# Kernel optimization log

Hardware: AMD Instinct MI355X
Metric: run time of the kernel (lower is better)

Reference implementation:

```python
import jax, jax.numpy as jnp
import numpy as np

FEA_DIM = 256
NUM_HEADS = 8
B, N = 32, 48


def setup_inputs() -> dict:
    key = jax.random.key(0)
    ks = jax.random.split(key, 30)
    d = FEA_DIM
    inp = {
        "async_fea": jax.random.normal(ks[0], (B, N, d), dtype=jnp.float32),
        "sync_fea": jax.random.normal(ks[1], (B, N, d), dtype=jnp.float32),
        "async_adj": jax.random.randint(ks[2], (B, N, N), 0, 2, dtype=jnp.int32),
        "sync_adj": jax.random.randint(ks[3], (B, N, N), 0, 2, dtype=jnp.int32),
    }
    i = 4
    for pref in ("a_", "s_"):
        for nm in ("Wq", "Wk", "Wv", "Wo", "Wm"):
            inp[pref + nm] = 0.02 * jax.random.normal(ks[i], (d, d), dtype=jnp.float32); i += 1
            inp[pref + nm.replace("W", "b")] = 0.02 * jax.random.normal(ks[i], (d,), dtype=jnp.float32); i += 1
    return inp


def _aggregate(x_src, adj, fallback, Wq, bq, Wk, bk, Wv, bv, Wo, bo, Wm, bm):
    """For each target t: self-attention among neighbor set {s : adj[b,s,t] > 0}
    of x_src, mean-pool over neighbors, divide by count again, linear map.
    Targets with no neighbors fall back to `fallback`."""
    Bb, Nn, D = x_src.shape
    H = NUM_HEADS
    dh = D // H
    q = (x_src @ Wq.T + bq).reshape(Bb, Nn, H, dh)
    k = (x_src @ Wk.T + bk).reshape(Bb, Nn, H, dh)
    v = (x_src @ Wv.T + bv).reshape(Bb, Nn, H, dh)
    # shared pairwise scores among source nodes: [B, H, Q, K]
    scores = jnp.einsum("bqhd,bkhd->bhqk", q, k) / jnp.sqrt(jnp.float32(dh))
    # neighbor mask per target: adj[b, s, t] > 0 -> m[b, t, s]
    m = jnp.transpose(adj > 0, (0, 2, 1))  # [B, T, S] bool
    # per-target masked softmax over keys: logits [B, T, H, Q, K]
    key_bias = jnp.where(m[:, :, None, None, :], 0.0, -1e9)
    attn = jax.nn.softmax(scores[:, None] + key_bias, axis=-1)  # [B,T,H,Q,K]
    out = jnp.einsum("bthqk,bkhd->bthqd", attn, v).reshape(Bb, Nn, Nn, D)  # [B,T,Q,D]
    out = out @ Wo.T + bo
    mf = m.astype(out.dtype)  # [B, T, Q]
    cnt = mf.sum(-1)  # [B, T]
    denom = jnp.maximum(cnt, 1.0)
    # torch: mean over valid queries, then / edge_cnt  => sum / cnt^2
    pooled = jnp.einsum("btq,btqd->btd", mf, out) / (denom * denom)[..., None]
    mapped = pooled @ Wm.T + bm
    return jnp.where((cnt > 0)[..., None], mapped, fallback)


def reference(async_fea, sync_fea, async_adj, sync_adj,
              a_Wq, a_bq, a_Wk, a_bk, a_Wv, a_bv, a_Wo, a_bo, a_Wm, a_bm,
              s_Wq, s_bq, s_Wk, s_bk, s_Wv, s_bv, s_Wo, s_bo, s_Wm, s_bm):
    refined_async = _aggregate(sync_fea, sync_adj, async_fea,
                               a_Wq, a_bq, a_Wk, a_bk, a_Wv, a_bv, a_Wo, a_bo, a_Wm, a_bm)
    refined_sync = _aggregate(async_fea, async_adj, sync_fea,
                              s_Wq, s_bq, s_Wk, s_bk, s_Wv, s_bv, s_Wo, s_bo, s_Wm, s_bm)
    return jnp.concatenate([refined_async, refined_sync, async_fea, sync_fea], axis=2)
```

## Files before the change

kernel.cpp:

```cpp
#include <hip/hip_runtime.h>

typedef __attribute__((ext_vector_type(8))) short short8v;
typedef __attribute__((ext_vector_type(4))) float f32x4;
typedef unsigned short u16t;

__device__ __forceinline__ u16t f2bf(float f) {
    union { float f; unsigned u; } v; v.f = f;
    unsigned u = v.u;
    return (u16t)((u + 0x7FFFu + ((u >> 16) & 1u)) >> 16);
}
__device__ __forceinline__ float bf2f(u16t u) {
    union { unsigned u; float f; } v; v.u = ((unsigned)u) << 16; return v.f;
}
__device__ __forceinline__ short8v cvt8(const float* p) {
    float4 lo = *(const float4*)p;
    float4 hi = *(const float4*)(p + 4);
    union { uint4 u; short8v s; } r;
    asm("v_cvt_pk_bf16_f32 %0, %1, %2" : "=v"(r.u.x) : "v"(lo.x), "v"(lo.y));
    asm("v_cvt_pk_bf16_f32 %0, %1, %2" : "=v"(r.u.y) : "v"(lo.z), "v"(lo.w));
    asm("v_cvt_pk_bf16_f32 %0, %1, %2" : "=v"(r.u.z) : "v"(hi.x), "v"(hi.y));
    asm("v_cvt_pk_bf16_f32 %0, %1, %2" : "=v"(r.u.w) : "v"(hi.z), "v"(hi.w));
    return r.s;
}
__device__ __forceinline__ short8v ld52(const u16t* p) {
    union { uint2 u[2]; short8v s; } r;
    r.u[0] = *(const uint2*)(p);
    r.u[1] = *(const uint2*)(p + 4);
    return r.s;
}

struct Params {
    const float *async_fea, *sync_fea;
    const int *async_adj, *sync_adj;
    const float *Wf[10];
    const float *bqkv[6];
    const float *bo_[2], *bm_[2];
    u16t *Wb;
    u16t *Qb, *Kb;
    u16t *VTg;
    u16t *Eg, *ETg;
    float *out;
};

__global__ __launch_bounds__(256) void convert_kernel(Params p)
{
    int g8 = (blockIdx.x * 256 + threadIdx.x) * 8;
    int w = g8 >> 16;
    int off = g8 & 65535;
    *(short8v*)(p.Wb + g8) = cvt8(p.Wf[w] + off);
}

__global__ __launch_bounds__(256) void qkv_kernel(Params p)
{
    int bid = blockIdx.x;
    int xcd = bid & 7, idx = bid >> 3;
    int agg = xcd >> 2, xcd_in = xcd & 3;
    int ct = idx % 12, rt = (idx / 12) * 4 + xcd_in;
    int wave = threadIdx.x >> 6, lane = threadIdx.x & 63;
    int l15 = lane & 15, g = lane >> 4;
    int row0 = rt * 64 + wave * 16;
    int mat = ct >> 2;
    int cbase = (ct & 3) * 64;
    const float* X = agg ? p.async_fea : p.sync_fea;
    const float* Xp = X + (row0 + l15) * 256 + g * 8;
    const u16t* Wp = p.Wb + (agg * 5 + mat) * 65536 + (cbase + l15) * 256 + g * 8;
    f32x4 acc[4] = {{0,0,0,0},{0,0,0,0},{0,0,0,0},{0,0,0,0}};
    #pragma unroll
    for (int kk = 0; kk < 8; ++kk) {
        short8v a = cvt8(Xp + kk * 32);
        #pragma unroll
        for (int j = 0; j < 4; ++j) {
            short8v b = *(const short8v*)(Wp + j * 16 * 256 + kk * 32);
            acc[j] = __builtin_amdgcn_mfma_f32_16x16x32_bf16(a, b, acc[j], 0, 0, 0);
        }
    }
    const float* bias = p.bqkv[agg * 3 + mat];
    if (mat < 2) {
        u16t* dst = ((mat == 0) ? p.Qb : p.Kb) + agg * 393216;
        #pragma unroll
        for (int j = 0; j < 4; ++j) {
            int c = cbase + j * 16 + l15;
            float bv = bias[c];
            #pragma unroll
            for (int i = 0; i < 4; ++i) {
                int row = row0 + g * 4 + i;
                dst[row * 256 + c] = f2bf(acc[j][i] + bv);
            }
        }
    } else {
        u16t* vt = p.VTg + agg * 393216;
        #pragma unroll
        for (int j = 0; j < 4; ++j) {
            int c = cbase + j * 16 + l15;
            float bv = bias[c];
            #pragma unroll
            for (int i = 0; i < 4; ++i) {
                int row = row0 + g * 4 + i;
                vt[(row / 48) * 12288 + c * 48 + (row % 48)] = f2bf(acc[j][i] + bv);
            }
        }
    }
}

__global__ __launch_bounds__(192) void scores_kernel(Params p)
{
    int bid = blockIdx.x;
    int xcd = bid & 7, idx = bid >> 3;
    int agg = xcd >> 2, xcd_in = xcd & 3;
    int h = idx & 7, b = (idx >> 3) * 4 + xcd_in;
    int qt = threadIdx.x >> 6, lane = threadIdx.x & 63;
    int l15 = lane & 15, g = lane >> 4;
    const u16t* Qp = p.Qb + agg * 393216 + (b * 48 + qt * 16 + l15) * 256 + h * 32 + g * 8;
    short8v a = *(const short8v*)Qp;
    f32x4 acc[3];
    #pragma unroll
    for (int kt = 0; kt < 3; ++kt) {
        const u16t* Kp = p.Kb + agg * 393216 + (b * 48 + kt * 16 + l15) * 256 + h * 32 + g * 8;
        short8v kb = *(const short8v*)Kp;
        f32x4 z = {0.f, 0.f, 0.f, 0.f};
        acc[kt] = __builtin_amdgcn_mfma_f32_16x16x32_bf16(a, kb, z, 0, 0, 0);
    }
    const float scale = 0.17677669529663687f;
    float sc[3][4], rm[4];
    #pragma unroll
    for (int i = 0; i < 4; ++i) {
        #pragma unroll
        for (int kt = 0; kt < 3; ++kt) sc[kt][i] = acc[kt][i] * scale;
        rm[i] = fmaxf(fmaxf(sc[0][i], sc[1][i]), sc[2][i]);
    }
    #pragma unroll
    for (int m = 1; m <= 8; m <<= 1)
        #pragma unroll
        for (int i = 0; i < 4; ++i) rm[i] = fmaxf(rm[i], __shfl_xor(rm[i], m));
    u16t* Eb  = p.Eg  + (agg * 32 + b) * 18432 + h * 2304;
    u16t* ETb = p.ETg + (agg * 32 + b) * 18432 + h * 2304;
    #pragma unroll
    for (int kt = 0; kt < 3; ++kt)
        #pragma unroll
        for (int i = 0; i < 4; ++i) {
            u16t ev = f2bf(__expf(sc[kt][i] - rm[i]));
            int q = qt * 16 + g * 4 + i, k = kt * 16 + l15;
            Eb[q * 48 + k]  = ev;
            ETb[k * 48 + q] = ev;
        }
}

#define IV_OFF   0
#define YV_OFF   13312
#define PL_OFF   26624
#define MSK_OFF  35072
#define CNT_OFF  36736
#define SM3_SIZE 36800
#define PO_OFF   IV_OFF
#define SP 52
#define XP 264

__global__ __launch_bounds__(512) void agg_kernel(Params p)
{
    __shared__ __attribute__((aligned(16))) char sm[SM3_SIZE];
    u16t* iv_  = (u16t*)(sm + IV_OFF);
    u16t* yv_  = (u16t*)(sm + YV_OFF);
    u16t* P_l  = (u16t*)(sm + PL_OFF);
    u16t* po_  = (u16t*)(sm + PO_OFF);
    u16t* mskb = (u16t*)(sm + MSK_OFF);
    float* cnt_l = (float*)(sm + CNT_OFF);

    const int bid = blockIdx.x, tid = threadIdx.x;
    const int xcd = bid & 7, idx = bid >> 3;
    const int agg = xcd >> 2, xcd_in = xcd & 3;
    const int tg = idx >> 3, b = ((idx & 7) << 2) | xcd_in;
    const int wave = tid >> 6, lane = tid & 63;
    const int l15 = lane & 15, g = lane >> 4;
    const int row_base = b * 48 + tg * 12;

    const float* fb  = agg ? p.sync_fea  : p.async_fea;
    const int*   adj = agg ? p.async_adj : p.sync_adj;
    const u16t* Egb  = p.Eg  + (agg * 32 + b) * 18432;
    const u16t* ETb  = p.ETg + (agg * 32 + b) * 18432;
    const u16t* VTb  = p.VTg + agg * 393216 + b * 12288;

    for (int e = tid; e < 16 * SP; e += 512) {
        int tt = e / SP, k = e - tt * SP;
        u16t v = 0;
        if (tt < 12 && k < 48)
            v = (adj[(b * 48 + k) * 48 + tg * 12 + tt] > 0) ? (u16t)0x3F80 : (u16t)0;
        mskb[e] = v;
    }
    {
        const float4* fb4 = (const float4*)fb;
        float4* out4 = (float4*)p.out;
        for (int e = tid; e < 768; e += 512) {
            int r = e >> 6, c = e & 63;
            out4[(row_base + r) * 256 + 128 + agg * 64 + c] =
                fb4[(row_base + r) * 64 + c];
        }
    }
    __syncthreads();
    if (tid < 12) {
        float c = 0.f;
        for (int s = 0; s < 48; ++s) c += bf2f(mskb[tid * SP + s]);
        cnt_l[tid] = c;
    }

    #pragma unroll
    for (int jj = 0; jj < 3; ++jj) {
        int rt = wave * 3 + jj;
        const u16t* Arow = Egb + (rt * 16 + l15) * 48;
        const u16t* Brow = mskb + l15 * SP;
        f32x4 acc = {0.f, 0.f, 0.f, 0.f};
        short8v a0 = *(const short8v*)(Arow + g * 8);
        short8v b0 = ld52(Brow + g * 8);
        acc = __builtin_amdgcn_mfma_f32_16x16x32_bf16(a0, b0, acc, 0, 0, 0);
        short8v a1 = {0,0,0,0,0,0,0,0}, b1 = {0,0,0,0,0,0,0,0};
        if (g < 2) { a1 = *(const short8v*)(Arow + 32 + g * 8); b1 = ld52(Brow + 32 + g * 8); }
        acc = __builtin_amdgcn_mfma_f32_16x16x32_bf16(a1, b1, acc, 0, 0, 0);
        #pragma unroll
        for (int i = 0; i < 4; ++i) {
            int row = rt * 16 + g * 4 + i;
            int h = row / 48, q = row - h * 48;
            float mq = bf2f(mskb[l15 * SP + q]);
            float ivv = (mq > 0.f) ? (1.f / acc[i]) : 0.f;
            iv_[(h * 16 + l15) * SP + q] = f2bf(ivv);
        }
    }
    __syncthreads();

    #pragma unroll
    for (int jj = 0; jj < 3; ++jj) {
        int job = wave * 3 + jj;
        int h = job / 3, kt = job % 3;
        const u16t* Arow = iv_ + (h * 16 + l15) * SP;
        const u16t* Brow = ETb + (h * 48 + kt * 16 + l15) * 48;
        f32x4 acc = {0.f, 0.f, 0.f, 0.f};
        short8v a0 = ld52(Arow + g * 8);
        short8v b0 = *(const short8v*)(Brow + g * 8);
        acc = __builtin_amdgcn_mfma_f32_16x16x32_bf16(a0, b0, acc, 0, 0, 0);
        short8v a1 = {0,0,0,0,0,0,0,0}, b1 = {0,0,0,0,0,0,0,0};
        if (g < 2) { a1 = ld52(Arow + 32 + g * 8); b1 = *(const short8v*)(Brow + 32 + g * 8); }
        acc = __builtin_amdgcn_mfma_f32_16x16x32_bf16(a1, b1, acc, 0, 0, 0);
        #pragma unroll
        for (int i = 0; i < 4; ++i) {
            int tt = g * 4 + i, k = kt * 16 + l15;
            float mk = bf2f(mskb[tt * SP + k]);
            yv_[(h * 16 + tt) * SP + k] = f2bf(acc[i] * mk);
        }
    }
    __syncthreads();

    #pragma unroll
    for (int jj = 0; jj < 2; ++jj) {
        int job = wave * 2 + jj;
        int h = job >> 1, dt = job & 1;
        const u16t* Arow = yv_ + (h * 16 + l15) * SP;
        const u16t* Brow = VTb + (h * 32 + dt * 16 + l15) * 48;
        f32x4 acc = {0.f, 0.f, 0.f, 0.f};
        short8v a0 = ld52(Arow + g * 8);
        short8v b0 = *(const short8v*)(Brow + g * 8);
        acc = __builtin_amdgcn_mfma_f32_16x16x32_bf16(a0, b0, acc, 0, 0, 0);
        short8v a1 = {0,0,0,0,0,0,0,0}, b1 = {0,0,0,0,0,0,0,0};
        if (g < 2) { a1 = ld52(Arow + 32 + g * 8); b1 = *(const short8v*)(Brow + 32 + g * 8); }
        acc = __builtin_amdgcn_mfma_f32_16x16x32_bf16(a1, b1, acc, 0, 0, 0);
        #pragma unroll
        for (int i = 0; i < 4; ++i)
            P_l[(g * 4 + i) * XP + h * 32 + dt * 16 + l15] = f2bf(acc[i]);
    }
    __syncthreads();

    {
        const u16t* Wo = p.Wb + (agg * 5 + 3) * 65536;
        const float* bo = p.bo_[agg];
        #pragma unroll
        for (int jj = 0; jj < 2; ++jj) {
            int ct = wave * 2 + jj;
            f32x4 acc = {0.f, 0.f, 0.f, 0.f};
            const u16t* Wp = Wo + (ct * 16 + l15) * 256 + g * 8;
            #pragma unroll
            for (int kk = 0; kk < 8; ++kk) {
                short8v a = *(const short8v*)(P_l + l15 * XP + kk * 32 + g * 8);
                short8v bf = *(const short8v*)(Wp + kk * 32);
                acc = __builtin_amdgcn_mfma_f32_16x16x32_bf16(a, bf, acc, 0, 0, 0);
            }
            int c = ct * 16 + l15;
            float bov = bo[c];
            #pragma unroll
            for (int i = 0; i < 4; ++i) {
                int t = g * 4 + i;
                float val = 0.f;
                if (t < 12) {
                    float cn = cnt_l[t];
                    float i1 = (cn > 0.f) ? 1.f / cn : 0.f;
                    val = acc[i] * i1 * i1 + bov * i1;
                }
                po_[t * XP + c] = f2bf(val);
            }
        }
    }
    __syncthreads();

    {
        const u16t* Wm = p.Wb + (agg * 5 + 4) * 65536;
        const float* bm = p.bm_[agg];
        #pragma unroll
        for (int jj = 0; jj < 2; ++jj) {
            int ct = wave * 2 + jj;
            f32x4 acc = {0.f, 0.f, 0.f, 0.f};
            const u16t* Wp = Wm + (ct * 16 + l15) * 256 + g * 8;
            #pragma unroll
            for (int kk = 0; kk < 8; ++kk) {
                short8v a = *(const short8v*)(po_ + l15 * XP + kk * 32 + g * 8);
                short8v bf = *(const short8v*)(Wp + kk * 32);
                acc = __builtin_amdgcn_mfma_f32_16x16x32_bf16(a, bf, acc, 0, 0, 0);
            }
            int c = ct * 16 + l15;
            float bmv = bm[c];
            #pragma unroll
            for (int i = 0; i < 4; ++i) {
                int t = g * 4 + i;
                if (t < 12) {
                    int grow = row_base + t;
                    float cn = cnt_l[t];
                    float val = (cn > 0.f) ? (acc[i] + bmv) : fb[grow * 256 + c];
                    p.out[grow * 1024 + agg * 256 + c] = val;
                }
            }
        }
    }
}

extern "C" void kernel_launch(void* const* d_in, const int* in_sizes, int n_in,
                              void* d_out, int out_size, void* d_ws, size_t ws_size,
                              hipStream_t stream)
{
    Params p;
    p.async_fea = (const float*)d_in[0];
    p.sync_fea  = (const float*)d_in[1];
    p.async_adj = (const int*)d_in[2];
    p.sync_adj  = (const int*)d_in[3];
    p.Wf[0] = (const float*)d_in[4];
    p.Wf[1] = (const float*)d_in[6];
    p.Wf[2] = (const float*)d_in[8];
    p.Wf[3] = (const float*)d_in[10];
    p.Wf[4] = (const float*)d_in[12];
    p.Wf[5] = (const float*)d_in[14];
    p.Wf[6] = (const float*)d_in[16];
    p.Wf[7] = (const float*)d_in[18];
    p.Wf[8] = (const float*)d_in[20];
    p.Wf[9] = (const float*)d_in[22];
    p.bqkv[0] = (const float*)d_in[5];
    p.bqkv[1] = (const float*)d_in[7];
    p.bqkv[2] = (const float*)d_in[9];
    p.bqkv[3] = (const float*)d_in[15];
    p.bqkv[4] = (const float*)d_in[17];
    p.bqkv[5] = (const float*)d_in[19];
    p.bo_[0] = (const float*)d_in[11];
    p.bo_[1] = (const float*)d_in[21];
    p.bm_[0] = (const float*)d_in[13];
    p.bm_[1] = (const float*)d_in[23];

    u16t* us = (u16t*)d_ws;
    p.Wb  = us;
    p.Qb  = p.Wb + 655360;
    p.Kb  = p.Qb + 786432;
    p.VTg = p.Kb + 786432;
    p.Eg  = p.VTg + 786432;
    p.ETg = p.Eg + 1179648;
    p.out = (float*)d_out;

    convert_kernel<<<320, 256, 0, stream>>>(p);
    qkv_kernel<<<576, 256, 0, stream>>>(p);
    scores_kernel<<<512, 192, 0, stream>>>(p);
    agg_kernel<<<256, 512, 0, stream>>>(p);
}
```

Baseline: 50.75 us.

## Fold Wo into Wm, drop weight-convert kernel, merge fold into QKV launch

Precomputes the combined weight Wc = Wm·Wo and bias Wm·bo in extra blocks of the QKV launch, so the aggregation kernel runs one 256x256 GEMM stage instead of two and loses a barrier. The separate fp32→bf16 weight-conversion kernel is removed: the QKV GEMM now converts weights inline from fp32. This cuts one launch and a GEMM stage per block. In exchange it adds fp32 weight reads in the QKV blocks and an extra rounding path through the bf16 folded weight.

```diff
diff --git a/kernel.cpp b/kernel.cpp
--- a/kernel.cpp
+++ b/kernel.cpp
@@ -32,72 +32,124 @@
 struct Params {
     const float *async_fea, *sync_fea;
     const int *async_adj, *sync_adj;
-    const float *Wf[10];
-    const float *bqkv[6];
-    const float *bo_[2], *bm_[2];
-    u16t *Wb;
+    const float *Wq[2], *Wk[2], *Wv[2];
+    const float *bq[2], *bk[2], *bv[2];
+    const float *Wo[2], *Wm[2], *bo_[2], *bm_[2];
     u16t *Qb, *Kb;
     u16t *VTg;
     u16t *Eg, *ETg;
+    u16t *Wcb;
+    float *bcw;
     float *out;
 };
 
-__global__ __launch_bounds__(256) void convert_kernel(Params p)
+__global__ __launch_bounds__(256) void qkv_fold(Params p)
 {
-    int g8 = (blockIdx.x * 256 + threadIdx.x) * 8;
-    int w = g8 >> 16;
-    int off = g8 & 65535;
-    *(short8v*)(p.Wb + g8) = cvt8(p.Wf[w] + off);
-}
-
-__global__ __launch_bounds__(256) void qkv_kernel(Params p)
-{
-    int bid = blockIdx.x;
-    int xcd = bid & 7, idx = bid >> 3;
-    int agg = xcd >> 2, xcd_in = xcd & 3;
-    int ct = idx % 12, rt = (idx / 12) * 4 + xcd_in;
-    int wave = threadIdx.x >> 6, lane = threadIdx.x & 63;
+    __shared__ float smem[2304];
+    int bid = blockIdx.x, tid = threadIdx.x;
+    int wave = tid >> 6, lane = tid & 63;
     int l15 = lane & 15, g = lane >> 4;
-    int row0 = rt * 64 + wave * 16;
-    int mat = ct >> 2;
-    int cbase = (ct & 3) * 64;
-    const float* X = agg ? p.async_fea : p.sync_fea;
-    const float* Xp = X + (row0 + l15) * 256 + g * 8;
-    const u16t* Wp = p.Wb + (agg * 5 + mat) * 65536 + (cbase + l15) * 256 + g * 8;
-    f32x4 acc[4] = {{0,0,0,0},{0,0,0,0},{0,0,0,0},{0,0,0,0}};
-    #pragma unroll
-    for (int kk = 0; kk < 8; ++kk) {
-        short8v a = cvt8(Xp + kk * 32);
-        #pragma unroll
-        for (int j = 0; j < 4; ++j) {
-            short8v b = *(const short8v*)(Wp + j * 16 * 256 + kk * 32);
-            acc[j] = __builtin_amdgcn_mfma_f32_16x16x32_bf16(a, b, acc[j], 0, 0, 0);
-        }
-    }
-    const float* bias = p.bqkv[agg * 3 + mat];
-    if (mat < 2) {
-        u16t* dst = ((mat == 0) ? p.Qb : p.Kb) + agg * 393216;
-        #pragma unroll
-        for (int j = 0; j < 4; ++j) {
-            int c = cbase + j * 16 + l15;
-            float bv = bias[c];
+
+    if (bid < 576) {
+        int xcd = bid & 7, idx = bid >> 3;
+        int agg = xcd >> 2, xcd_in = xcd & 3;
+        int ct = idx % 12, rt = (idx / 12) * 4 + xcd_in;
+        int row0 = rt * 64 + wave * 16;
+        int mat = ct >> 2;
+        int cbase = (ct & 3) * 64;
+        const float* X = agg ? p.async_fea : p.sync_fea;
+        const float* W    = (mat == 0) ? p.Wq[agg] : (mat == 1) ? p.Wk[agg] : p.Wv[agg];
+        const float* bias = (mat == 0) ? p.bq[agg] : (mat == 1) ? p.bk[agg] : p.bv[agg];
+        const float* Xp = X + (row0 + l15) * 256 + g * 8;
+        const float* Wp = W + (cbase + l15) * 256 + g * 8;
+        f32x4 acc[4] = {{0,0,0,0},{0,0,0,0},{0,0,0,0},{0,0,0,0}};
+        #pragma unroll
+        for (int kk = 0; kk < 8; ++kk) {
+            short8v a = cvt8(Xp + kk * 32);
+            #pragma unroll
+            for (int j = 0; j < 4; ++j) {
+                short8v b = cvt8(Wp + j * 16 * 256 + kk * 32);
+                acc[j] = __builtin_amdgcn_mfma_f32_16x16x32_bf16(a, b, acc[j], 0, 0, 0);
+            }
+        }
+        if (mat < 2) {
+            u16t* dst = ((mat == 0) ? p.Qb : p.Kb) + agg * 393216;
+            #pragma unroll
+            for (int j = 0; j < 4; ++j) {
+                int c = cbase + j * 16 + l15;
+                float bv = bias[c];
+                #pragma unroll
+                for (int i = 0; i < 4; ++i) {
+                    int row = row0 + g * 4 + i;
+                    dst[row * 256 + c] = f2bf(acc[j][i] + bv);
+                }
+            }
+        } else {
+            u16t* vt = p.VTg + agg * 393216;
+            #pragma unroll
+            for (int j = 0; j < 4; ++j) {
+                int c = cbase + j * 16 + l15;
+                float bv = bias[c];
+                #pragma unroll
+                for (int i = 0; i < 4; ++i) {
+                    int row = row0 + g * 4 + i;
+                    vt[(row / 48) * 12288 + c * 48 + (row % 48)] = f2bf(acc[j][i] + bv);
+                }
+            }
+        }
+    } else {
+        int fid = bid - 576;
+        int agg = fid >> 4, tile = fid & 15;
+        int cb = (tile >> 2) * 64, db = (tile & 3) * 64;
+        const float* Wm = p.Wm[agg];
+        const float* Wo = p.Wo[agg];
+        const float* bo = p.bo_[agg];
+        u16t* Wcb = p.Wcb + agg * 65536;
+        float* bc = p.bcw + agg * 256;
+        int crow = cb + wave * 16 + l15;
+        const float* Wmp = Wm + crow * 256 + g * 8;
+        f32x4 acc[4] = {{0,0,0,0},{0,0,0,0},{0,0,0,0},{0,0,0,0}};
+        for (int ch = 0; ch < 8; ++ch) {
+            __syncthreads();
+            #pragma unroll
+            for (int l = 0; l < 8; ++l) {
+                int e = l * 256 + tid;
+                int ii = e >> 6, dd = e & 63;
+                smem[dd * 36 + ii] = Wo[(ch * 32 + ii) * 256 + db + dd];
+            }
+            __syncthreads();
+            short8v a = cvt8(Wmp + ch * 32);
+            #pragma unroll
+            for (int j = 0; j < 4; ++j) {
+                float* sp = &smem[(j * 16 + l15) * 36 + g * 8];
+                float4 lo = *(const float4*)sp;
+                float4 hi = *(const float4*)(sp + 4);
+                union { uint4 u; short8v s; } rb;
+                asm("v_cvt_pk_bf16_f32 %0, %1, %2" : "=v"(rb.u.x) : "v"(lo.x), "v"(lo.y));
+                asm("v_cvt_pk_bf16_f32 %0, %1, %2" : "=v"(rb.u.y) : "v"(lo.z), "v"(lo.w));
+                asm("v_cvt_pk_bf16_f32 %0, %1, %2" : "=v"(rb.u.z) : "v"(hi.x), "v"(hi.y));
+                asm("v_cvt_pk_bf16_f32 %0, %1, %2" : "=v"(rb.u.w) : "v"(hi.z), "v"(hi.w));
+                acc[j] = __builtin_amdgcn_mfma_f32_16x16x32_bf16(a, rb.s, acc[j], 0, 0, 0);
+            }
+        }
+        #pragma unroll
+        for (int j = 0; j < 4; ++j)
             #pragma unroll
             for (int i = 0; i < 4; ++i) {
-                int row = row0 + g * 4 + i;
-                dst[row * 256 + c] = f2bf(acc[j][i] + bv);
-            }
-        }
-    } else {
-        u16t* vt = p.VTg + agg * 393216;
-        #pragma unroll
-        for (int j = 0; j < 4; ++j) {
-            int c = cbase + j * 16 + l15;
-            float bv = bias[c];
-            #pragma unroll
-            for (int i = 0; i < 4; ++i) {
-                int row = row0 + g * 4 + i;
-                vt[(row / 48) * 12288 + c * 48 + (row % 48)] = f2bf(acc[j][i] + bv);
-            }
+                int c = cb + wave * 16 + g * 4 + i;
+                int d = db + j * 16 + l15;
+                Wcb[c * 256 + d] = f2bf(acc[j][i]);
+            }
+        if ((tile & 3) == 0) {
+            int r = tid >> 2, s = tid & 3;
+            const float* wmr = Wm + (cb + r) * 256 + s * 64;
+            const float* bor = bo + s * 64;
+            float a = 0.f;
+            #pragma unroll
+            for (int i = 0; i < 64; ++i) a += wmr[i] * bor[i];
+            a += __shfl_xor(a, 1);
+            a += __shfl_xor(a, 2);
+            if (s == 0) bc[cb + r] = a;
         }
     }
 }
@@ -151,7 +203,6 @@
 #define MSK_OFF  35072
 #define CNT_OFF  36736
 #define SM3_SIZE 36800
-#define PO_OFF   IV_OFF
 #define SP 52
 #define XP 264
 
@@ -161,7 +212,6 @@
     u16t* iv_  = (u16t*)(sm + IV_OFF);
     u16t* yv_  = (u16t*)(sm + YV_OFF);
     u16t* P_l  = (u16t*)(sm + PL_OFF);
-    u16t* po_  = (u16t*)(sm + PO_OFF);
     u16t* mskb = (u16t*)(sm + MSK_OFF);
     float* cnt_l = (float*)(sm + CNT_OFF);
 
@@ -267,13 +317,14 @@
     __syncthreads();
 
     {
-        const u16t* Wo = p.Wb + (agg * 5 + 3) * 65536;
-        const float* bo = p.bo_[agg];
+        const u16t* Wc = p.Wcb + agg * 65536;
+        const float* bc = p.bcw + agg * 256;
+        const float* bm = p.bm_[agg];
         #pragma unroll
         for (int jj = 0; jj < 2; ++jj) {
             int ct = wave * 2 + jj;
             f32x4 acc = {0.f, 0.f, 0.f, 0.f};
-            const u16t* Wp = Wo + (ct * 16 + l15) * 256 + g * 8;
+            const u16t* Wp = Wc + (ct * 16 + l15) * 256 + g * 8;
             #pragma unroll
             for (int kk = 0; kk < 8; ++kk) {
                 short8v a = *(const short8v*)(P_l + l15 * XP + kk * 32 + g * 8);
@@ -281,45 +332,20 @@
                 acc = __builtin_amdgcn_mfma_f32_16x16x32_bf16(a, bf, acc, 0, 0, 0);
             }
             int c = ct * 16 + l15;
-            float bov = bo[c];
-            #pragma unroll
-            for (int i = 0; i < 4; ++i) {
-                int t = g * 4 + i;
-                float val = 0.f;
-                if (t < 12) {
-                    float cn = cnt_l[t];
-                    float i1 = (cn > 0.f) ? 1.f / cn : 0.f;
-                    val = acc[i] * i1 * i1 + bov * i1;
-                }
-                po_[t * XP + c] = f2bf(val);
-            }
-        }
-    }
-    __syncthreads();
-
-    {
-        const u16t* Wm = p.Wb + (agg * 5 + 4) * 65536;
-        const float* bm = p.bm_[agg];
-        #pragma unroll
-        for (int jj = 0; jj < 2; ++jj) {
-            int ct = wave * 2 + jj;
-            f32x4 acc = {0.f, 0.f, 0.f, 0.f};
-            const u16t* Wp = Wm + (ct * 16 + l15) * 256 + g * 8;
-            #pragma unroll
-            for (int kk = 0; kk < 8; ++kk) {
-                short8v a = *(const short8v*)(po_ + l15 * XP + kk * 32 + g * 8);
-                short8v bf = *(const short8v*)(Wp + kk * 32);
-                acc = __builtin_amdgcn_mfma_f32_16x16x32_bf16(a, bf, acc, 0, 0, 0);
-            }
-            int c = ct * 16 + l15;
-            float bmv = bm[c];
+            float bcv = bc[c], bmv = bm[c];
             #pragma unroll
             for (int i = 0; i < 4; ++i) {
                 int t = g * 4 + i;
                 if (t < 12) {
                     int grow = row_base + t;
                     float cn = cnt_l[t];
-                    float val = (cn > 0.f) ? (acc[i] + bmv) : fb[grow * 256 + c];
+                    float val;
+                    if (cn > 0.f) {
+                        float i1 = 1.f / cn;
+                        val = acc[i] * i1 * i1 + bcv * i1 + bmv;
+                    } else {
+                        val = fb[grow * 256 + c];
+                    }
                     p.out[grow * 1024 + agg * 256 + c] = val;
                 }
             }
@@ -336,38 +362,28 @@
     p.sync_fea  = (const float*)d_in[1];
     p.async_adj = (const int*)d_in[2];
     p.sync_adj  = (const int*)d_in[3];
-    p.Wf[0] = (const float*)d_in[4];
-    p.Wf[1] = (const float*)d_in[6];
-    p.Wf[2] = (const float*)d_in[8];
-    p.Wf[3] = (const float*)d_in[10];
-    p.Wf[4] = (const float*)d_in[12];
-    p.Wf[5] = (const float*)d_in[14];
-    p.Wf[6] = (const float*)d_in[16];
-    p.Wf[7] = (const float*)d_in[18];
-    p.Wf[8] = (const float*)d_in[20];
-    p.Wf[9] = (const float*)d_in[22];
-    p.bqkv[0] = (const float*)d_in[5];
-    p.bqkv[1] = (const float*)d_in[7];
-    p.bqkv[2] = (const float*)d_in[9];
-    p.bqkv[3] = (const float*)d_in[15];
-    p.bqkv[4] = (const float*)d_in[17];
-    p.bqkv[5] = (const float*)d_in[19];
-    p.bo_[0] = (const float*)d_in[11];
-    p.bo_[1] = (const float*)d_in[21];
-    p.bm_[0] = (const float*)d_in[13];
-    p.bm_[1] = (const float*)d_in[23];
+    p.Wq[0] = (const float*)d_in[4];   p.bq[0] = (const float*)d_in[5];
+    p.Wk[0] = (const float*)d_in[6];   p.bk[0] = (const float*)d_in[7];
+    p.Wv[0] = (const float*)d_in[8];   p.bv[0] = (const float*)d_in[9];
+    p.Wo[0] = (const float*)d_in[10];  p.bo_[0] = (const float*)d_in[11];
+    p.Wm[0] = (const float*)d_in[12];  p.bm_[0] = (const float*)d_in[13];
+    p.Wq[1] = (const float*)d_in[14];  p.bq[1] = (const float*)d_in[15];
+    p.Wk[1] = (const float*)d_in[16];  p.bk[1] = (const float*)d_in[17];
+    p.Wv[1] = (const float*)d_in[18];  p.bv[1] = (const float*)d_in[19];
+    p.Wo[1] = (const float*)d_in[20];  p.bo_[1] = (const float*)d_in[21];
+    p.Wm[1] = (const float*)d_in[22];  p.bm_[1] = (const float*)d_in[23];
 
     u16t* us = (u16t*)d_ws;
-    p.Wb  = us;
-    p.Qb  = p.Wb + 655360;
+    p.Qb  = us;
     p.Kb  = p.Qb + 786432;
     p.VTg = p.Kb + 786432;
     p.Eg  = p.VTg + 786432;
     p.ETg = p.Eg + 1179648;
+    p.Wcb = p.ETg + 1179648;
+    p.bcw = (float*)(p.Wcb + 131072);
     p.out = (float*)d_out;
 
-    convert_kernel<<<320, 256, 0, stream>>>(p);
-    qkv_kernel<<<576, 256, 0, stream>>>(p);
+    qkv_fold<<<608, 256, 0, stream>>>(p);
     scores_kernel<<<512, 192, 0, stream>>>(p);
     agg_kernel<<<256, 512, 0, stream>>>(p);
 }
```

New measurement: 52.48 us. 1.03x slower.
